# Kernel tuning notes

Measured on AMD Instinct MI355X. Metric: run time of the kernel, lower is better.

The kernel has to match this reference:

```python
import jax, jax.numpy as jnp
import numpy as np

N_NODES = 10000
N_EDGES = 320000
IN_F, H1, H2 = 512, 256, 64


def setup_inputs() -> dict:
    key = jax.random.key(0)
    ks = jax.random.split(key, 8)
    x = jax.random.normal(ks[0], (N_NODES, IN_F), dtype=jnp.float32)
    edge_src = jax.random.randint(ks[1], (N_EDGES,), 0, N_NODES, dtype=jnp.int32)
    edge_dst = jax.random.randint(ks[2], (N_EDGES,), 0, N_NODES, dtype=jnp.int32)
    edge_weight = jax.random.uniform(ks[3], (N_EDGES,), dtype=jnp.float32)
    # Glorot-initialized GCN weights + biases
    W1 = jax.random.normal(ks[4], (IN_F, H1), dtype=jnp.float32) * (1.0 / np.sqrt(IN_F))
    b1 = jnp.zeros((H1,), dtype=jnp.float32)
    W2 = jax.random.normal(ks[5], (H1, H2), dtype=jnp.float32) * (1.0 / np.sqrt(H1))
    b2 = jnp.zeros((H2,), dtype=jnp.float32)
    return {"x": x, "W1": W1, "b1": b1, "W2": W2, "b2": b2,
            "edge_weight": edge_weight, "edge_src": edge_src, "edge_dst": edge_dst}


def _gcn_layer(h, W, b, edge_src, edge_dst, edge_weight, act):
    # support = h @ W  (dropout is identity in eval mode)
    support = h @ W  # [N, out]
    # sparse adjacency aggregation: out[dst] += w * support[src]
    msgs = support[edge_src] * edge_weight[:, None]  # [E, out]
    agg = jax.ops.segment_sum(msgs, edge_dst, num_segments=h.shape[0])
    return act(agg + b)


def reference(x, W1, b1, W2, b2, edge_weight, edge_src, edge_dst):
    h1 = _gcn_layer(x, W1, b1, edge_src, edge_dst, edge_weight, jax.nn.relu)
    z = _gcn_layer(h1, W2, b2, edge_src, edge_dst, edge_weight, jax.nn.relu)  # embeddings
    # InnerProductDecoder: sigmoid(z @ z.T)
    recon = jax.nn.sigmoid(z @ z.T)  # [N, N]
    return (z, recon)
```

## Files before the change

kernel.cpp:

```cpp
#include <hip/hip_runtime.h>

#define N_NODES 10000
#define N_EDGES 320000
#define IN_F    512
#define H1F     256
#define H2F     64

typedef __attribute__((ext_vector_type(8)))  short short8;
typedef __attribute__((ext_vector_type(16))) float f32x16;

__device__ __forceinline__ unsigned short f2bf(float f) {
    union { float fl; unsigned int i; } v; v.fl = f;
    unsigned int x = v.i;
    return (unsigned short)((x + 0x7fffu + ((x >> 16) & 1u)) >> 16);
}
__device__ __forceinline__ float bf2f(unsigned short u) {
    union { unsigned int i; float f; } v; v.i = ((unsigned int)u) << 16; return v.f;
}

__global__ __launch_bounds__(1024) void k_classify(const int* __restrict__ c0,
                                                   const int* __restrict__ c2,
                                                   int* __restrict__ sel,
                                                   int* __restrict__ deg) {
    __shared__ int cnt0, cnt2;
    int t = threadIdx.x;
    if (t == 0) { cnt0 = 0; cnt2 = 0; }
    for (int i = t; i < N_NODES; i += 1024) deg[i] = 0;
    __syncthreads();
    int v0 = c0[t];
    int v2 = c2[t];
    if (v0 >= 0 && v0 < N_NODES) atomicAdd(&cnt0, 1);
    if (v2 >= 0 && v2 < N_NODES) atomicAdd(&cnt2, 1);
    __syncthreads();
    if (t == 0) *sel = (cnt0 > 900 && cnt2 <= 900) ? 1 : 0;
}

__global__ __launch_bounds__(256) void k_hist(const int* __restrict__ c0,
                                              const int* __restrict__ c2,
                                              const int* __restrict__ sel,
                                              int* __restrict__ deg) {
    int e = blockIdx.x * 256 + threadIdx.x;
    if (e >= N_EDGES) return;
    int dst = (*sel) ? c0[e] : c2[e];
    if ((unsigned)dst < N_NODES) atomicAdd(&deg[dst], 1);
}

__global__ __launch_bounds__(1024) void k_scan(const int* __restrict__ deg,
                                               int* __restrict__ off,
                                               int* __restrict__ cursor) {
    __shared__ int part[1024];
    int t = threadIdx.x;
    const int chunk = (N_NODES + 1023) / 1024;
    int begin = t * chunk;
    int end = begin + chunk; if (end > N_NODES) end = N_NODES;
    if (begin > N_NODES) begin = N_NODES;
    int s = 0;
    for (int i = begin; i < end; ++i) s += deg[i];
    part[t] = s;
    __syncthreads();
    for (int o = 1; o < 1024; o <<= 1) {
        int v = (t >= o) ? part[t - o] : 0;
        __syncthreads();
        part[t] += v;
        __syncthreads();
    }
    int base = (t == 0) ? 0 : part[t - 1];
    for (int i = begin; i < end; ++i) {
        off[i] = base; cursor[i] = base; base += deg[i];
    }
    if (t == 1023) off[N_NODES] = part[1023];
}

__global__ __launch_bounds__(256) void k_bucket(const int* __restrict__ c0,
                                                const int* __restrict__ c1,
                                                const int* __restrict__ c2,
                                                const float* __restrict__ c0f,
                                                const float* __restrict__ c2f,
                                                const int* __restrict__ sel,
                                                int* __restrict__ cursor,
                                                int* __restrict__ srcp,
                                                float* __restrict__ wp) {
    int e = blockIdx.x * 256 + threadIdx.x;
    if (e >= N_EDGES) return;
    int s = *sel;
    int src = c1[e];
    int dst = s ? c0[e] : c2[e];
    float w = s ? c2f[e] : c0f[e];
    if ((unsigned)src >= N_NODES || (unsigned)dst >= N_NODES) return;
    int p = atomicAdd(&cursor[dst], 1);
    srcp[p] = src;
    wp[p] = w;
}

__global__ __launch_bounds__(256) void k_gemm1(const float* __restrict__ x,
                                               const float* __restrict__ W1,
                                               unsigned short* __restrict__ sup1b) {
    __shared__ float xs[IN_F][8];
    int nb = blockIdx.x * 8;
    int t = threadIdx.x;
    {
        int n  = t & 7;
        int k0 = (t >> 3) * 16;
        const float* xr = x + (size_t)(nb + n) * IN_F + k0;
        #pragma unroll
        for (int c = 0; c < 16; c += 4) {
            float4 v = *(const float4*)(xr + c);
            xs[k0 + c + 0][n] = v.x;
            xs[k0 + c + 1][n] = v.y;
            xs[k0 + c + 2][n] = v.z;
            xs[k0 + c + 3][n] = v.w;
        }
    }
    __syncthreads();
    int f = t;
    float acc[8] = {0.f,0.f,0.f,0.f,0.f,0.f,0.f,0.f};
    #pragma unroll 8
    for (int k = 0; k < IN_F; ++k) {
        float w = W1[(size_t)k * H1F + f];
        float4 a = *(const float4*)&xs[k][0];
        float4 b = *(const float4*)&xs[k][4];
        acc[0] += a.x * w; acc[1] += a.y * w; acc[2] += a.z * w; acc[3] += a.w * w;
        acc[4] += b.x * w; acc[5] += b.y * w; acc[6] += b.z * w; acc[7] += b.w * w;
    }
    #pragma unroll
    for (int n = 0; n < 8; ++n)
        sup1b[(size_t)(nb + n) * H1F + f] = f2bf(acc[n]);
}

__global__ __launch_bounds__(256) void k_agg1(const unsigned short* __restrict__ sup1b,
                                              const int* __restrict__ off,
                                              const int* __restrict__ srcp,
                                              const float* __restrict__ wp,
                                              const float* __restrict__ b1,
                                              float* __restrict__ h1) {
    int node = blockIdx.x;
    int f = threadIdx.x;
    int s = off[node], e = off[node + 1];
    float acc = 0.f;
    for (int i = s; i < e; ++i) {
        float w = wp[i];
        int src = srcp[i];
        acc += w * bf2f(sup1b[(size_t)src * H1F + f]);
    }
    h1[(size_t)node * H1F + f] = fmaxf(acc + b1[f], 0.f);
}

__global__ __launch_bounds__(64) void k_gemm2(const float* __restrict__ h1,
                                              const float* __restrict__ W2,
                                              float* __restrict__ sup2) {
    __shared__ float hs[H1F][4];
    int nb = blockIdx.x * 4;
    int t = threadIdx.x;
    {
        int n  = t & 3;
        int k0 = (t >> 2) * 16;
        const float* hr = h1 + (size_t)(nb + n) * H1F + k0;
        #pragma unroll
        for (int c = 0; c < 16; c += 4) {
            float4 v = *(const float4*)(hr + c);
            hs[k0 + c + 0][n] = v.x;
            hs[k0 + c + 1][n] = v.y;
            hs[k0 + c + 2][n] = v.z;
            hs[k0 + c + 3][n] = v.w;
        }
    }
    __syncthreads();
    int f = t;
    float acc[4] = {0.f,0.f,0.f,0.f};
    #pragma unroll 8
    for (int k = 0; k < H1F; ++k) {
        float w = W2[(size_t)k * H2F + f];
        float4 a = *(const float4*)&hs[k][0];
        acc[0] += a.x * w; acc[1] += a.y * w; acc[2] += a.z * w; acc[3] += a.w * w;
    }
    #pragma unroll
    for (int n = 0; n < 4; ++n)
        sup2[(size_t)(nb + n) * H2F + f] = acc[n];
}

__global__ __launch_bounds__(64) void k_agg2(const float* __restrict__ sup2,
                                             const int* __restrict__ off,
                                             const int* __restrict__ srcp,
                                             const float* __restrict__ wp,
                                             const float* __restrict__ b2,
                                             float* __restrict__ zout,
                                             unsigned short* __restrict__ zb) {
    int node = blockIdx.x;
    int f = threadIdx.x;
    int s = off[node], e = off[node + 1];
    float acc = 0.f;
    for (int i = s; i < e; ++i) {
        float w = wp[i];
        int src = srcp[i];
        acc += w * sup2[(size_t)src * H2F + f];
    }
    acc = fmaxf(acc + b2[f], 0.f);
    zout[(size_t)node * H2F + f] = acc;
    zb[(size_t)node * H2F + f] = f2bf(acc);
}

__global__ __launch_bounds__(256) void k_decoder(const unsigned short* __restrict__ zb,
                                                 float* __restrict__ recon) {
    int t = threadIdx.x;
    int wave = t >> 6, lane = t & 63;
    int i0 = blockIdx.y * 64 + (wave >> 1) * 32;
    int j0 = blockIdx.x * 64 + (wave & 1) * 32;
    int r = lane & 31, half = lane >> 5;
    int arow = i0 + r, brow = j0 + r;

    short8 zero8 = {0,0,0,0,0,0,0,0};
    short8 a[4], b[4];
    #pragma unroll
    for (int s = 0; s < 4; ++s) {
        a[s] = (arow < N_NODES) ? *(const short8*)(zb + (size_t)arow * H2F + s * 16 + half * 8)
                                : zero8;
        b[s] = (brow < N_NODES) ? *(const short8*)(zb + (size_t)brow * H2F + s * 16 + half * 8)
                                : zero8;
    }

    f32x16 acc;
    #pragma unroll
    for (int i = 0; i < 16; ++i) acc[i] = 0.f;
    #pragma unroll
    for (int s = 0; s < 4; ++s)
        acc = __builtin_amdgcn_mfma_f32_32x32x16_bf16(a[s], b[s], acc, 0, 0, 0);

    #pragma unroll
    for (int rg = 0; rg < 16; ++rg) {
        int row = i0 + (rg & 3) + 8 * (rg >> 2) + 4 * half;
        int col = j0 + r;
        if (row < N_NODES && col < N_NODES) {
            float sv = acc[rg];
            recon[(size_t)row * N_NODES + col] = 1.0f / (1.0f + __expf(-sv));
        }
    }
}

extern "C" void kernel_launch(void* const* d_in, const int* in_sizes, int n_in,
                              void* d_out, int out_size, void* d_ws, size_t ws_size,
                              hipStream_t stream) {
    int ix = -1, iW1 = -1, ib1 = -1, iW2 = -1, ib2 = -1, ic0 = -1, ic1 = -1, ic2 = -1;
    for (int i = 0; i < n_in; ++i) {
        int s = in_sizes[i];
        if      (s == N_NODES * IN_F) ix = i;
        else if (s == IN_F * H1F)     iW1 = i;
        else if (s == H1F)            ib1 = i;
        else if (s == H1F * H2F)      iW2 = i;
        else if (s == H2F)            ib2 = i;
        else if (s == N_EDGES) { if (ic0 < 0) ic0 = i; else if (ic1 < 0) ic1 = i; else ic2 = i; }
    }
    if (ix < 0 || iW1 < 0 || ib1 < 0 || iW2 < 0 || ib2 < 0 || ic0 < 0 || ic1 < 0 || ic2 < 0) {
        ix = 0; iW1 = 1; ib1 = 2; iW2 = 3; ib2 = 4; ic0 = 5; ic1 = 6; ic2 = 7;
    }
    const float* x  = (const float*)d_in[ix];
    const float* W1 = (const float*)d_in[iW1];
    const float* b1 = (const float*)d_in[ib1];
    const float* W2 = (const float*)d_in[iW2];
    const float* b2 = (const float*)d_in[ib2];
    const int*   c0  = (const int*)d_in[ic0];
    const int*   c1  = (const int*)d_in[ic1];
    const int*   c2  = (const int*)d_in[ic2];
    const float* c0f = (const float*)d_in[ic0];
    const float* c2f = (const float*)d_in[ic2];

    float* zout  = (float*)d_out;
    float* recon = zout + (size_t)N_NODES * H2F;

    unsigned short* zb = (unsigned short*)d_ws;

    char* scratch = (char*)recon;
    size_t o = 0;
    auto alloc = [&](size_t bytes) { size_t p = o; o += (bytes + 255) & ~(size_t)255; return p; };
    int*            sel    = (int*)           (scratch + alloc(256));
    int*            deg    = (int*)           (scratch + alloc((size_t)N_NODES * 4));
    int*            off    = (int*)           (scratch + alloc((size_t)(N_NODES + 1) * 4));
    int*            cursor = (int*)           (scratch + alloc((size_t)N_NODES * 4));
    int*            srcp   = (int*)           (scratch + alloc((size_t)N_EDGES * 4));
    float*          wp     = (float*)         (scratch + alloc((size_t)N_EDGES * 4));
    unsigned short* sup1b  = (unsigned short*)(scratch + alloc((size_t)N_NODES * H1F * 2));
    float*          h1     = (float*)         (scratch + alloc((size_t)N_NODES * H1F * 4));
    float*          sup2   = (float*)         (scratch + alloc((size_t)N_NODES * H2F * 4));

    k_classify<<<1, 1024, 0, stream>>>(c0, c2, sel, deg);
    k_hist  <<<(N_EDGES + 255) / 256, 256, 0, stream>>>(c0, c2, sel, deg);
    k_scan  <<<1, 1024, 0, stream>>>(deg, off, cursor);
    k_bucket<<<(N_EDGES + 255) / 256, 256, 0, stream>>>(c0, c1, c2, c0f, c2f, sel, cursor, srcp, wp);

    k_gemm1<<<N_NODES / 8, 256, 0, stream>>>(x, W1, sup1b);
    k_agg1 <<<N_NODES, 256, 0, stream>>>(sup1b, off, srcp, wp, b1, h1);

    k_gemm2<<<N_NODES / 4, 64, 0, stream>>>(h1, W2, sup2);
    k_agg2 <<<N_NODES, 64, 0, stream>>>(sup2, off, srcp, wp, b2, zout, zb);

    dim3 dgrid((N_NODES + 63) / 64, (N_NODES + 63) / 64);
    k_decoder<<<dgrid, 256, 0, stream>>>(zb, recon);
}
```

Measured before the change: 655.5 us.

## Pack edge src/weight into int2, stage edges in LDS, unroll aggregation

Replaces the single-block classify kernel with a per-edge check that decides which input buffer holds the destination (an int in range means it is an index rather than a float weight), and zeroes degrees with a memset. Source index and weight are packed into one int2 array. The aggregation kernels stage edge chunks in shared memory and use four independent accumulators so several gathers can be in flight at once. The per-edge heuristic assumes float weights never look like valid indices, and the extra barriers add a small overhead per chunk.

```diff
diff --git a/kernel.cpp b/kernel.cpp
--- a/kernel.cpp
+++ b/kernel.cpp
@@ -18,30 +18,17 @@
     union { unsigned int i; float f; } v; v.i = ((unsigned int)u) << 16; return v.f;
 }
 
-__global__ __launch_bounds__(1024) void k_classify(const int* __restrict__ c0,
-                                                   const int* __restrict__ c2,
-                                                   int* __restrict__ sel,
-                                                   int* __restrict__ deg) {
-    __shared__ int cnt0, cnt2;
-    int t = threadIdx.x;
-    if (t == 0) { cnt0 = 0; cnt2 = 0; }
-    for (int i = t; i < N_NODES; i += 1024) deg[i] = 0;
-    __syncthreads();
-    int v0 = c0[t];
-    int v2 = c2[t];
-    if (v0 >= 0 && v0 < N_NODES) atomicAdd(&cnt0, 1);
-    if (v2 >= 0 && v2 < N_NODES) atomicAdd(&cnt2, 1);
-    __syncthreads();
-    if (t == 0) *sel = (cnt0 > 900 && cnt2 <= 900) ? 1 : 0;
+__device__ __forceinline__ bool edge_is_alpha(int a0) {
+    return (unsigned)a0 < N_NODES;
 }
 
 __global__ __launch_bounds__(256) void k_hist(const int* __restrict__ c0,
                                               const int* __restrict__ c2,
-                                              const int* __restrict__ sel,
                                               int* __restrict__ deg) {
     int e = blockIdx.x * 256 + threadIdx.x;
     if (e >= N_EDGES) return;
-    int dst = (*sel) ? c0[e] : c2[e];
+    int a0 = c0[e];
+    int dst = edge_is_alpha(a0) ? a0 : c2[e];
     if ((unsigned)dst < N_NODES) atomicAdd(&deg[dst], 1);
 }
 
@@ -76,20 +63,18 @@
                                                 const int* __restrict__ c2,
                                                 const float* __restrict__ c0f,
                                                 const float* __restrict__ c2f,
-                                                const int* __restrict__ sel,
                                                 int* __restrict__ cursor,
-                                                int* __restrict__ srcp,
-                                                float* __restrict__ wp) {
+                                                int2* __restrict__ ep) {
     int e = blockIdx.x * 256 + threadIdx.x;
     if (e >= N_EDGES) return;
-    int s = *sel;
+    int a0 = c0[e];
+    bool alpha = edge_is_alpha(a0);
     int src = c1[e];
-    int dst = s ? c0[e] : c2[e];
-    float w = s ? c2f[e] : c0f[e];
+    int dst = alpha ? a0 : c2[e];
+    float w = alpha ? c2f[e] : c0f[e];
     if ((unsigned)src >= N_NODES || (unsigned)dst >= N_NODES) return;
     int p = atomicAdd(&cursor[dst], 1);
-    srcp[p] = src;
-    wp[p] = w;
+    ep[p] = make_int2(src, __float_as_int(w));
 }
 
 __global__ __launch_bounds__(256) void k_gemm1(const float* __restrict__ x,
@@ -129,19 +114,33 @@
 
 __global__ __launch_bounds__(256) void k_agg1(const unsigned short* __restrict__ sup1b,
                                               const int* __restrict__ off,
-                                              const int* __restrict__ srcp,
-                                              const float* __restrict__ wp,
+                                              const int2* __restrict__ ep,
                                               const float* __restrict__ b1,
                                               float* __restrict__ h1) {
+    __shared__ int2 eds[256];
     int node = blockIdx.x;
     int f = threadIdx.x;
     int s = off[node], e = off[node + 1];
-    float acc = 0.f;
-    for (int i = s; i < e; ++i) {
-        float w = wp[i];
-        int src = srcp[i];
-        acc += w * bf2f(sup1b[(size_t)src * H1F + f]);
-    }
+    float a0 = 0.f, a1 = 0.f, a2 = 0.f, a3 = 0.f;
+    for (int base = s; base < e; base += 256) {
+        int n = e - base; if (n > 256) n = 256;
+        __syncthreads();
+        if (f < n) eds[f] = ep[base + f];
+        __syncthreads();
+        int j = 0;
+        for (; j + 4 <= n; j += 4) {
+            int2 e0 = eds[j], e1 = eds[j+1], e2 = eds[j+2], e3 = eds[j+3];
+            a0 += __int_as_float(e0.y) * bf2f(sup1b[(size_t)e0.x * H1F + f]);
+            a1 += __int_as_float(e1.y) * bf2f(sup1b[(size_t)e1.x * H1F + f]);
+            a2 += __int_as_float(e2.y) * bf2f(sup1b[(size_t)e2.x * H1F + f]);
+            a3 += __int_as_float(e3.y) * bf2f(sup1b[(size_t)e3.x * H1F + f]);
+        }
+        for (; j < n; ++j) {
+            int2 e0 = eds[j];
+            a0 += __int_as_float(e0.y) * bf2f(sup1b[(size_t)e0.x * H1F + f]);
+        }
+    }
+    float acc = (a0 + a1) + (a2 + a3);
     h1[(size_t)node * H1F + f] = fmaxf(acc + b1[f], 0.f);
 }
 
@@ -180,20 +179,34 @@
 
 __global__ __launch_bounds__(64) void k_agg2(const float* __restrict__ sup2,
                                              const int* __restrict__ off,
-                                             const int* __restrict__ srcp,
-                                             const float* __restrict__ wp,
+                                             const int2* __restrict__ ep,
                                              const float* __restrict__ b2,
                                              float* __restrict__ zout,
                                              unsigned short* __restrict__ zb) {
+    __shared__ int2 eds[64];
     int node = blockIdx.x;
     int f = threadIdx.x;
     int s = off[node], e = off[node + 1];
-    float acc = 0.f;
-    for (int i = s; i < e; ++i) {
-        float w = wp[i];
-        int src = srcp[i];
-        acc += w * sup2[(size_t)src * H2F + f];
-    }
+    float a0 = 0.f, a1 = 0.f, a2 = 0.f, a3 = 0.f;
+    for (int base = s; base < e; base += 64) {
+        int n = e - base; if (n > 64) n = 64;
+        __syncthreads();
+        if (f < n) eds[f] = ep[base + f];
+        __syncthreads();
+        int j = 0;
+        for (; j + 4 <= n; j += 4) {
+            int2 e0 = eds[j], e1 = eds[j+1], e2 = eds[j+2], e3 = eds[j+3];
+            a0 += __int_as_float(e0.y) * sup2[(size_t)e0.x * H2F + f];
+            a1 += __int_as_float(e1.y) * sup2[(size_t)e1.x * H2F + f];
+            a2 += __int_as_float(e2.y) * sup2[(size_t)e2.x * H2F + f];
+            a3 += __int_as_float(e3.y) * sup2[(size_t)e3.x * H2F + f];
+        }
+        for (; j < n; ++j) {
+            int2 e0 = eds[j];
+            a0 += __int_as_float(e0.y) * sup2[(size_t)e0.x * H2F + f];
+        }
+    }
+    float acc = (a0 + a1) + (a2 + a3);
     acc = fmaxf(acc + b2[f], 0.f);
     zout[(size_t)node * H2F + f] = acc;
     zb[(size_t)node * H2F + f] = f2bf(acc);
@@ -271,26 +284,24 @@
     char* scratch = (char*)recon;
     size_t o = 0;
     auto alloc = [&](size_t bytes) { size_t p = o; o += (bytes + 255) & ~(size_t)255; return p; };
-    int*            sel    = (int*)           (scratch + alloc(256));
     int*            deg    = (int*)           (scratch + alloc((size_t)N_NODES * 4));
     int*            off    = (int*)           (scratch + alloc((size_t)(N_NODES + 1) * 4));
     int*            cursor = (int*)           (scratch + alloc((size_t)N_NODES * 4));
-    int*            srcp   = (int*)           (scratch + alloc((size_t)N_EDGES * 4));
-    float*          wp     = (float*)         (scratch + alloc((size_t)N_EDGES * 4));
+    int2*           ep     = (int2*)          (scratch + alloc((size_t)N_EDGES * 8));
     unsigned short* sup1b  = (unsigned short*)(scratch + alloc((size_t)N_NODES * H1F * 2));
     float*          h1     = (float*)         (scratch + alloc((size_t)N_NODES * H1F * 4));
     float*          sup2   = (float*)         (scratch + alloc((size_t)N_NODES * H2F * 4));
 
-    k_classify<<<1, 1024, 0, stream>>>(c0, c2, sel, deg);
-    k_hist  <<<(N_EDGES + 255) / 256, 256, 0, stream>>>(c0, c2, sel, deg);
+    hipMemsetAsync(deg, 0, (size_t)N_NODES * 4, stream);
+    k_hist  <<<(N_EDGES + 255) / 256, 256, 0, stream>>>(c0, c2, deg);
     k_scan  <<<1, 1024, 0, stream>>>(deg, off, cursor);
-    k_bucket<<<(N_EDGES + 255) / 256, 256, 0, stream>>>(c0, c1, c2, c0f, c2f, sel, cursor, srcp, wp);
+    k_bucket<<<(N_EDGES + 255) / 256, 256, 0, stream>>>(c0, c1, c2, c0f, c2f, cursor, ep);
 
     k_gemm1<<<N_NODES / 8, 256, 0, stream>>>(x, W1, sup1b);
-    k_agg1 <<<N_NODES, 256, 0, stream>>>(sup1b, off, srcp, wp, b1, h1);
+    k_agg1 <<<N_NODES, 256, 0, stream>>>(sup1b, off, ep, b1, h1);
 
     k_gemm2<<<N_NODES / 4, 64, 0, stream>>>(h1, W2, sup2);
-    k_agg2 <<<N_NODES, 64, 0, stream>>>(sup2, off, srcp, wp, b2, zout, zb);
+    k_agg2 <<<N_NODES, 64, 0, stream>>>(sup2, off, ep, b2, zout, zb);
 
     dim3 dgrid((N_NODES + 63) / 64, (N_NODES + 63) / 64);
     k_decoder<<<dgrid, 256, 0, stream>>>(zb, recon);
```

New measurement: 611.6 us. 6.7% less time.
